# Performance work log

Measured on AMD Instinct MI355X. Metric: run time of the kernel, lower is better.

The kernel has to match this reference:

```python
import jax, jax.numpy as jnp
import numpy as np

DISCRETIZATION = "IM"  # matches init_kwargs


def setup_inputs() -> dict:
    key = jax.random.key(0)
    ks = jax.random.split(key, 6)
    Bt, L, H, P = 16, 4096, 128, 256
    std = 1.0 / np.sqrt(H)
    return {
        "inputs": jax.random.normal(ks[0], (Bt, L, H), jnp.float32),
        "A_diag": jax.random.uniform(ks[1], (P,), jnp.float32, 0.0, 1.0),
        "B": jax.random.uniform(ks[2], (P, H, 2), jnp.float32, -std, std),
        "C": jax.random.uniform(ks[3], (H, P, 2), jnp.float32, -std, std),
        "D": jax.random.normal(ks[4], (H,), jnp.float32),
        "steps": jax.random.uniform(ks[5], (P,), jnp.float32, 0.0, 1.0),
    }


def _combine(l, r):
    # 2x2 block composition: new_A = r.A @ l.A ; new_b = r.A @ l.b + r.b
    la11, la12, la21, la22, lb1, lb2 = l
    ra11, ra12, ra21, ra22, rb1, rb2 = r
    c11 = ra11 * la11 + ra12 * la21
    c12 = ra11 * la12 + ra12 * la22
    c21 = ra21 * la11 + ra22 * la21
    c22 = ra21 * la12 + ra22 * la22
    nb1 = ra11 * lb1 + ra12 * lb2 + rb1
    nb2 = ra21 * lb1 + ra22 * lb2 + rb2
    return (c11, c12, c21, c22, nb1, nb2)


def reference(inputs, A_diag, B, C, D, steps):
    Bt, L, H = inputs.shape
    P = A_diag.shape[0]
    a = jax.nn.relu(A_diag)                 # (P,)
    step = jax.nn.sigmoid(steps)            # (P,)
    Bc = jax.lax.complex(B[..., 0], B[..., 1])   # (P, H) complex64
    Cc = jax.lax.complex(C[..., 0], C[..., 1])   # (H, P) complex64

    # bu = inputs @ B^T  -> (Bt, L, P), complex
    bu = jnp.einsum("blh,ph->blp", inputs.astype(jnp.complex64), Bc)

    if DISCRETIZATION == "IM":
        s2a = step * step * a
        schur = 1.0 / (1.0 + s2a)
        m11 = 1.0 - s2a * schur
        m12 = -step * a * schur
        m21 = step * schur
        m22 = schur
        f1 = (m11 * step) * bu
        f2 = (m21 * step) * bu
    else:  # IMEX
        m11 = jnp.ones_like(a)
        m12 = -step * a
        m21 = step
        m22 = 1.0 - step * step * a
        f1 = bu * step
        f2 = bu * (step * step)

    # sequence axis leading for the scan: (L, Bt, P)
    f1 = jnp.moveaxis(f1, 1, 0)
    f2 = jnp.moveaxis(f2, 1, 0)
    # time-invariant 2x2 per-channel blocks, broadcast to (L, 1, P) complex
    a_elems = tuple(
        jnp.broadcast_to(m.astype(jnp.complex64)[None, None, :], (L, 1, P))
        for m in (m11, m12, m21, m22)
    )
    _, _, _, _, _x1, x2 = jax.lax.associative_scan(
        _combine, (*a_elems, f1, f2), axis=0
    )
    states = x2  # (L, Bt, P): position component (index 1 of 2x2 state)

    projected = jnp.einsum("lbp,hp->blh", states, Cc).real  # (Bt, L, H)
    return projected + inputs * D
```

## Files before the change

kernel.cpp:

```cpp
#include <hip/hip_runtime.h>
#include <math.h>


constexpr int BTc = 16;
constexpr int Lc  = 4096;
constexpr int Hc  = 128;
constexpr int Pc  = 256;
constexpr int CL  = 64;
constexpr int NC  = Lc / CL;
constexpr int LOG2CL = 6;

typedef __attribute__((ext_vector_type(8))) short short8;
typedef __attribute__((ext_vector_type(4))) float f32x4;

constexpr size_t CF_OFF  = 0;
constexpr size_t BF_OFF  = 16384;
constexpr size_t CFR_OFF = BF_OFF + 131072;
constexpr size_t LOC_OFF = CFR_OFF + 131072;
constexpr size_t INI_OFF = LOC_OFF + 4194304;

constexpr int LDS_U   = 0;
constexpr int LDS_BUX = 16384;
constexpr int LDS_BYTES = 81920;

__device__ __forceinline__ unsigned short f2bf(float x) {
    unsigned u = __float_as_uint(x);
    u += 0x7fffu + ((u >> 16) & 1u);
    return (unsigned short)(u >> 16);
}
__device__ __forceinline__ float bf2f(unsigned short h) {
    return __uint_as_float(((unsigned)h) << 16);
}
__device__ __forceinline__ f32x4 mfma16(short8 a, short8 b, f32x4 c) {
    return __builtin_amdgcn_mfma_f32_16x16x32_bf16(a, b, c, 0, 0, 0);
}
__device__ __forceinline__ int swz(int l) { return (l ^ (l >> 3)) & 7; }

__global__ __launch_bounds__(256) void k_prep(const float* __restrict__ A_diag,
                                              const float* __restrict__ steps,
                                              const float* __restrict__ Bw,
                                              const float* __restrict__ Cw,
                                              float* __restrict__ cf,
                                              unsigned short* __restrict__ BF,
                                              unsigned short* __restrict__ CFr) {
    int idx = blockIdx.x * 256 + threadIdx.x;
    {
        int j = idx & 7, lane = (idx >> 3) & 63, nfg = (idx >> 9) & 31, kt = idx >> 14;
        int k = kt * 32 + (lane >> 4) * 8 + j;
        int n = nfg * 16 + (lane & 15);
        int p = n >> 1, part = n & 1;
        BF[idx] = f2bf(Bw[(p * Hc + k) * 2 + part]);
    }
    {
        int j = idx & 7, lane = (idx >> 3) & 63, nfg = (idx >> 9) & 7, ktG = idx >> 12;
        int k = ktG * 32 + (lane >> 4) * 8 + j;
        int h = nfg * 16 + (lane & 15);
        int p = k >> 1, part = k & 1;
        float v = Cw[(h * Pc + p) * 2 + part];
        CFr[idx] = f2bf(part ? -v : v);
    }
    if (blockIdx.x == 0) {
        int p = threadIdx.x;
        float a  = fmaxf(A_diag[p], 0.0f);
        float st = 1.0f / (1.0f + expf(-steps[p]));
        float s2a   = st * st * a;
        float schur = 1.0f / (1.0f + s2a);
        float m11 = 1.0f - s2a * schur;
        float m12 = -st * a * schur;
        float m21 = st * schur;
        float m22 = schur;
        cf[0*Pc+p] = m11;  cf[1*Pc+p] = m12;
        cf[2*Pc+p] = m21;  cf[3*Pc+p] = m22;
        cf[4*Pc+p] = m11 * st;
        cf[5*Pc+p] = m21 * st;
        float a11=m11, a12=m12, a21=m21, a22=m22;
        #pragma unroll
        for (int i = 0; i < LOG2CL; i++) {
            float b11 = a11*a11 + a12*a21;
            float b12 = a11*a12 + a12*a22;
            float b21 = a21*a11 + a22*a21;
            float b22 = a21*a12 + a22*a22;
            a11=b11; a12=b12; a21=b21; a22=b22;
        }
        cf[6*Pc+p]=a11; cf[7*Pc+p]=a12; cf[8*Pc+p]=a21; cf[9*Pc+p]=a22;
    }
}

__global__ __launch_bounds__(512) void k_scanB(const float* __restrict__ cf,
                                               const float2* __restrict__ loc,
                                               float2* __restrict__ ini) {
    int b = blockIdx.x, n = threadIdx.x;
    int p = n >> 1;
    float A11=cf[6*Pc+p], A12=cf[7*Pc+p], A21=cf[8*Pc+p], A22=cf[9*Pc+p];
    float x1 = 0.f, x2 = 0.f;
    for (int g = 0; g < 8; g++) {
        float2 lv[8];
        #pragma unroll
        for (int j = 0; j < 8; j++)
            lv[j] = loc[((size_t)(b * NC + g * 8 + j)) * 512 + n];
        #pragma unroll
        for (int j = 0; j < 8; j++) {
            size_t idx = ((size_t)(b * NC + g * 8 + j)) * 512 + n;
            ini[idx] = make_float2(x1, x2);
            float n1 = fmaf(A11, x1, fmaf(A12, x2, lv[j].x));
            float n2 = fmaf(A21, x1, fmaf(A22, x2, lv[j].y));
            x1 = n1; x2 = n2;
        }
    }
}

template<int PASS>
__global__ __launch_bounds__(512, 4) void k_pass(const float* __restrict__ in,
                                                 const float* __restrict__ cf,
                                                 const unsigned short* __restrict__ BF,
                                                 const unsigned short* __restrict__ CFr,
                                                 const float* __restrict__ Dw,
                                                 float2* __restrict__ loc,
                                                 const float2* __restrict__ ini,
                                                 float* __restrict__ out) {
    __shared__ float4 smem4[LDS_BYTES / 16];
    char* sm = (char*)smem4;

    int tid  = threadIdx.x;
    int lane = tid & 63;
    int w    = tid >> 6;
    int wm   = w >> 2, wn = w & 3;
    int bc   = blockIdx.x;
    size_t mbase = (size_t)bc * CL;
    int r = lane & 15, q = lane >> 4;

    {
        int l   = tid >> 3;
        int kc0 = (tid & 7) * 2;
        const float* g = in + (mbase + l) * Hc + (tid & 7) * 16;
        float4 f0 = *(const float4*)(g);
        float4 f1 = *(const float4*)(g + 4);
        float4 f2 = *(const float4*)(g + 8);
        float4 f3 = *(const float4*)(g + 12);
        short8 c0, c1;
        c0[0]=(short)f2bf(f0.x); c0[1]=(short)f2bf(f0.y); c0[2]=(short)f2bf(f0.z); c0[3]=(short)f2bf(f0.w);
        c0[4]=(short)f2bf(f1.x); c0[5]=(short)f2bf(f1.y); c0[6]=(short)f2bf(f1.z); c0[7]=(short)f2bf(f1.w);
        c1[0]=(short)f2bf(f2.x); c1[1]=(short)f2bf(f2.y); c1[2]=(short)f2bf(f2.z); c1[3]=(short)f2bf(f2.w);
        c1[4]=(short)f2bf(f3.x); c1[5]=(short)f2bf(f3.y); c1[6]=(short)f2bf(f3.z); c1[7]=(short)f2bf(f3.w);
        int sw = l & 7;
        *(short8*)(sm + LDS_U + l * 256 + (((kc0    ) ^ sw) << 4)) = c0;
        *(short8*)(sm + LDS_U + l * 256 + (((kc0 + 1) ^ sw) << 4)) = c1;
    }
    __syncthreads();

    #pragma unroll
    for (int half = 0; half < 2; ++half) {
        f32x4 acc[2][4];
        #pragma unroll
        for (int i = 0; i < 2; i++)
            #pragma unroll
            for (int j = 0; j < 4; j++) acc[i][j] = (f32x4)(0.0f);

        #pragma unroll
        for (int kt = 0; kt < 4; ++kt) {
            short8 a[2];
            #pragma unroll
            for (int mf = 0; mf < 2; ++mf) {
                int la = wm * 32 + mf * 16 + r;
                int kc = kt * 4 + q;
                a[mf] = *(const short8*)(sm + LDS_U + la * 256 + ((kc ^ (la & 7)) << 4));
            }
            #pragma unroll
            for (int nfi = 0; nfi < 4; ++nfi) {
                int nfg = half * 16 + wn * 4 + nfi;
                short8 bb = *(const short8*)(BF + (size_t)((kt * 32 + nfg) * 64 + lane) * 8);
                acc[0][nfi] = mfma16(a[0], bb, acc[0][nfi]);
                acc[1][nfi] = mfma16(a[1], bb, acc[1][nfi]);
            }
        }
        char* bux = sm + LDS_BUX + half * 32768;
        #pragma unroll
        for (int mf = 0; mf < 2; ++mf)
            #pragma unroll
            for (int nfi = 0; nfi < 4; ++nfi) {
                int nn = wn * 64 + nfi * 16 + r;
                int kc = nn >> 3, e = nn & 7;
                #pragma unroll
                for (int j = 0; j < 4; ++j) {
                    int l = wm * 32 + mf * 16 + q * 4 + j;
                    *(unsigned short*)(bux + l * 512 + ((kc ^ swz(l)) << 4) + e * 2)
                        = f2bf(acc[mf][nfi][j]);
                }
            }
    }
    __syncthreads();

    {
        int ng = tid, h = ng >> 8, n = ng & 255, p = ng >> 1;
        float m11 = cf[p],        m12 = cf[256 + p];
        float m21 = cf[512 + p],  m22 = cf[768 + p];
        float s1  = cf[1024 + p], s2  = cf[1280 + p];
        float x1, x2;
        if constexpr (PASS == 1) { x1 = 0.f; x2 = 0.f; }
        else { float2 iv = ini[(size_t)bc * 512 + ng]; x1 = iv.x; x2 = iv.y; }
        char* bux = sm + LDS_BUX + h * 32768 + (n & 7) * 2;
        int kc = n >> 3;
        #pragma unroll 4
        for (int l = 0; l < CL; ++l) {
            char* addr = bux + l * 512 + ((kc ^ swz(l)) << 4);
            float f  = bf2f(*(unsigned short*)addr);
            float n1 = fmaf(m11, x1, fmaf(m12, x2, s1 * f));
            float n2 = fmaf(m21, x1, fmaf(m22, x2, s2 * f));
            x1 = n1; x2 = n2;
            if constexpr (PASS == 2) *(unsigned short*)addr = f2bf(x2);
        }
        if constexpr (PASS == 1) loc[(size_t)bc * 512 + ng] = make_float2(x1, x2);
    }

    if constexpr (PASS == 2) {
        __syncthreads();
        f32x4 acc2[2][2];
        #pragma unroll
        for (int i = 0; i < 2; i++)
            #pragma unroll
            for (int j = 0; j < 2; j++) acc2[i][j] = (f32x4)(0.0f);

        #pragma unroll
        for (int half = 0; half < 2; ++half) {
            char* bux = sm + LDS_BUX + half * 32768;
            #pragma unroll
            for (int kt = 0; kt < 8; ++kt) {
                short8 a2[2];
                #pragma unroll
                for (int mf = 0; mf < 2; ++mf) {
                    int la  = wm * 32 + mf * 16 + r;
                    int kc2 = kt * 4 + q;
                    a2[mf] = *(const short8*)(bux + la * 512 + ((kc2 ^ swz(la)) << 4));
                }
                #pragma unroll
                for (int nfi = 0; nfi < 2; ++nfi) {
                    int ktG = half * 8 + kt;
                    int nfg = wn * 2 + nfi;
                    short8 bb = *(const short8*)(CFr + (size_t)((ktG * 8 + nfg) * 64 + lane) * 8);
                    acc2[0][nfi] = mfma16(a2[0], bb, acc2[0][nfi]);
                    acc2[1][nfi] = mfma16(a2[1], bb, acc2[1][nfi]);
                }
            }
        }
        #pragma unroll
        for (int nfi = 0; nfi < 2; ++nfi) {
            int h = wn * 32 + nfi * 16 + r;
            float d = Dw[h];
            #pragma unroll
            for (int mf = 0; mf < 2; ++mf)
                #pragma unroll
                for (int j = 0; j < 4; ++j) {
                    int l = wm * 32 + mf * 16 + q * 4 + j;
                    size_t gm = mbase + l;
                    out[gm * Hc + h] = fmaf(in[gm * Hc + h], d, acc2[mf][nfi][j]);
                }
        }
    }
}

extern "C" void kernel_launch(void* const* d_in, const int* in_sizes, int n_in,
                              void* d_out, int out_size, void* d_ws, size_t ws_size,
                              hipStream_t stream) {
    const float* in  = (const float*)d_in[0];
    const float* Ad  = (const float*)d_in[1];
    const float* Bw  = (const float*)d_in[2];
    const float* Cw  = (const float*)d_in[3];
    const float* Dw  = (const float*)d_in[4];
    const float* stp = (const float*)d_in[5];
    char* ws = (char*)d_ws;
    float*          cf  = (float*)(ws + CF_OFF);
    unsigned short* BF  = (unsigned short*)(ws + BF_OFF);
    unsigned short* CFr = (unsigned short*)(ws + CFR_OFF);
    float2*         loc = (float2*)(ws + LOC_OFF);
    float2*         ini = (float2*)(ws + INI_OFF);
    float* out = (float*)d_out;

    k_prep<<<256, 256, 0, stream>>>(Ad, stp, Bw, Cw, cf, BF, CFr);
    k_pass<1><<<BTc * NC, 512, 0, stream>>>(in, cf, BF, CFr, Dw, loc, ini, out);
    k_scanB<<<BTc, 512, 0, stream>>>(cf, loc, ini);
    k_pass<2><<<BTc * NC, 512, 0, stream>>>(in, cf, BF, CFr, Dw, loc, ini, out);
}
```

Measured before the change: 150.9 us.

## Replace first-pass sequential chunk scan with weighted-sum reduction and halve pass-two LDS

```diff
diff --git a/kernel.cpp b/kernel.cpp
--- a/kernel.cpp
+++ b/kernel.cpp
@@ -15,13 +15,16 @@
 
 constexpr size_t CF_OFF  = 0;
 constexpr size_t BF_OFF  = 16384;
-constexpr size_t CFR_OFF = BF_OFF + 131072;
-constexpr size_t LOC_OFF = CFR_OFF + 131072;
+constexpr size_t CFR_OFF = BF_OFF  + 131072;
+constexpr size_t W_OFF   = CFR_OFF + 131072;
+constexpr size_t LOC_OFF = W_OFF   + 131072;
 constexpr size_t INI_OFF = LOC_OFF + 4194304;
 
 constexpr int LDS_U   = 0;
 constexpr int LDS_BUX = 16384;
-constexpr int LDS_BYTES = 81920;
+constexpr int LDS2_BYTES = 49152;
+constexpr int LDS_PART = 16384;
+constexpr int LDSS_BYTES = 20480;
 
 __device__ __forceinline__ unsigned short f2bf(float x) {
     unsigned u = __float_as_uint(x);
@@ -42,7 +45,8 @@
                                               const float* __restrict__ Cw,
                                               float* __restrict__ cf,
                                               unsigned short* __restrict__ BF,
-                                              unsigned short* __restrict__ CFr) {
+                                              unsigned short* __restrict__ CFr,
+                                              float2* __restrict__ W) {
     int idx = blockIdx.x * 256 + threadIdx.x;
     {
         int j = idx & 7, lane = (idx >> 3) & 63, nfg = (idx >> 9) & 31, kt = idx >> 14;
@@ -71,8 +75,16 @@
         float m22 = schur;
         cf[0*Pc+p] = m11;  cf[1*Pc+p] = m12;
         cf[2*Pc+p] = m21;  cf[3*Pc+p] = m22;
-        cf[4*Pc+p] = m11 * st;
-        cf[5*Pc+p] = m21 * st;
+        float s1 = m11 * st, s2 = m21 * st;
+        cf[4*Pc+p] = s1;
+        cf[5*Pc+p] = s2;
+        float w1 = s1, w2 = s2;
+        for (int k = 0; k < CL; k++) {
+            W[p * CL + k] = make_float2(w1, w2);
+            float t1 = fmaf(m11, w1, m12 * w2);
+            float t2 = fmaf(m21, w1, m22 * w2);
+            w1 = t1; w2 = t2;
+        }
         float a11=m11, a12=m12, a21=m21, a22=m22;
         #pragma unroll
         for (int i = 0; i < LOG2CL; i++) {
@@ -109,17 +121,59 @@
     }
 }
 
-template<int PASS>
-__global__ __launch_bounds__(512, 4) void k_pass(const float* __restrict__ in,
-                                                 const float* __restrict__ cf,
-                                                 const unsigned short* __restrict__ BF,
-                                                 const unsigned short* __restrict__ CFr,
-                                                 const float* __restrict__ Dw,
-                                                 float2* __restrict__ loc,
-                                                 const float2* __restrict__ ini,
-                                                 float* __restrict__ out) {
-    __shared__ float4 smem4[LDS_BYTES / 16];
+__device__ __forceinline__ void stage_U(char* sm, const float* __restrict__ in,
+                                        size_t mbase, int tid) {
+    int l   = tid >> 3;
+    int kc0 = (tid & 7) * 2;
+    const float* g = in + (mbase + l) * Hc + (tid & 7) * 16;
+    float4 f0 = *(const float4*)(g);
+    float4 f1 = *(const float4*)(g + 4);
+    float4 f2 = *(const float4*)(g + 8);
+    float4 f3 = *(const float4*)(g + 12);
+    short8 c0, c1;
+    c0[0]=(short)f2bf(f0.x); c0[1]=(short)f2bf(f0.y); c0[2]=(short)f2bf(f0.z); c0[3]=(short)f2bf(f0.w);
+    c0[4]=(short)f2bf(f1.x); c0[5]=(short)f2bf(f1.y); c0[6]=(short)f2bf(f1.z); c0[7]=(short)f2bf(f1.w);
+    c1[0]=(short)f2bf(f2.x); c1[1]=(short)f2bf(f2.y); c1[2]=(short)f2bf(f2.z); c1[3]=(short)f2bf(f2.w);
+    c1[4]=(short)f2bf(f3.x); c1[5]=(short)f2bf(f3.y); c1[6]=(short)f2bf(f3.z); c1[7]=(short)f2bf(f3.w);
+    int sw = l & 7;
+    *(short8*)(sm + LDS_U + l * 256 + (((kc0    ) ^ sw) << 4)) = c0;
+    *(short8*)(sm + LDS_U + l * 256 + (((kc0 + 1) ^ sw) << 4)) = c1;
+}
+
+__device__ __forceinline__ void gemm1_half(char* sm, const unsigned short* __restrict__ BF,
+                                           int half, int wm, int wn, int lane,
+                                           f32x4 (&acc)[2][4]) {
+    int r = lane & 15, q = lane >> 4;
+    #pragma unroll
+    for (int i = 0; i < 2; i++)
+        #pragma unroll
+        for (int j = 0; j < 4; j++) acc[i][j] = (f32x4)(0.0f);
+    #pragma unroll
+    for (int kt = 0; kt < 4; ++kt) {
+        short8 a[2];
+        #pragma unroll
+        for (int mf = 0; mf < 2; ++mf) {
+            int la = wm * 32 + mf * 16 + r;
+            int kc = kt * 4 + q;
+            a[mf] = *(const short8*)(sm + LDS_U + la * 256 + ((kc ^ (la & 7)) << 4));
+        }
+        #pragma unroll
+        for (int nfi = 0; nfi < 4; ++nfi) {
+            int nfg = half * 16 + wn * 4 + nfi;
+            short8 bb = *(const short8*)(BF + (size_t)((kt * 32 + nfg) * 64 + lane) * 8);
+            acc[0][nfi] = mfma16(a[0], bb, acc[0][nfi]);
+            acc[1][nfi] = mfma16(a[1], bb, acc[1][nfi]);
+        }
+    }
+}
+
+__global__ __launch_bounds__(512, 6) void k_sum(const float* __restrict__ in,
+                                                const unsigned short* __restrict__ BF,
+                                                const float2* __restrict__ W,
+                                                float2* __restrict__ loc) {
+    __shared__ float4 smem4[LDSS_BYTES / 16];
     char* sm = (char*)smem4;
+    float2* part = (float2*)(sm + LDS_PART);
 
     int tid  = threadIdx.x;
     int lane = tid & 63;
@@ -129,51 +183,85 @@
     size_t mbase = (size_t)bc * CL;
     int r = lane & 15, q = lane >> 4;
 
-    {
-        int l   = tid >> 3;
-        int kc0 = (tid & 7) * 2;
-        const float* g = in + (mbase + l) * Hc + (tid & 7) * 16;
-        float4 f0 = *(const float4*)(g);
-        float4 f1 = *(const float4*)(g + 4);
-        float4 f2 = *(const float4*)(g + 8);
-        float4 f3 = *(const float4*)(g + 12);
-        short8 c0, c1;
-        c0[0]=(short)f2bf(f0.x); c0[1]=(short)f2bf(f0.y); c0[2]=(short)f2bf(f0.z); c0[3]=(short)f2bf(f0.w);
-        c0[4]=(short)f2bf(f1.x); c0[5]=(short)f2bf(f1.y); c0[6]=(short)f2bf(f1.z); c0[7]=(short)f2bf(f1.w);
-        c1[0]=(short)f2bf(f2.x); c1[1]=(short)f2bf(f2.y); c1[2]=(short)f2bf(f2.z); c1[3]=(short)f2bf(f2.w);
-        c1[4]=(short)f2bf(f3.x); c1[5]=(short)f2bf(f3.y); c1[6]=(short)f2bf(f3.z); c1[7]=(short)f2bf(f3.w);
-        int sw = l & 7;
-        *(short8*)(sm + LDS_U + l * 256 + (((kc0    ) ^ sw) << 4)) = c0;
-        *(short8*)(sm + LDS_U + l * 256 + (((kc0 + 1) ^ sw) << 4)) = c1;
-    }
+    stage_U(sm, in, mbase, tid);
     __syncthreads();
 
     #pragma unroll
     for (int half = 0; half < 2; ++half) {
         f32x4 acc[2][4];
-        #pragma unroll
-        for (int i = 0; i < 2; i++)
-            #pragma unroll
-            for (int j = 0; j < 4; j++) acc[i][j] = (f32x4)(0.0f);
-
-        #pragma unroll
-        for (int kt = 0; kt < 4; ++kt) {
-            short8 a[2];
-            #pragma unroll
-            for (int mf = 0; mf < 2; ++mf) {
-                int la = wm * 32 + mf * 16 + r;
-                int kc = kt * 4 + q;
-                a[mf] = *(const short8*)(sm + LDS_U + la * 256 + ((kc ^ (la & 7)) << 4));
-            }
-            #pragma unroll
-            for (int nfi = 0; nfi < 4; ++nfi) {
-                int nfg = half * 16 + wn * 4 + nfi;
-                short8 bb = *(const short8*)(BF + (size_t)((kt * 32 + nfg) * 64 + lane) * 8);
-                acc[0][nfi] = mfma16(a[0], bb, acc[0][nfi]);
-                acc[1][nfi] = mfma16(a[1], bb, acc[1][nfi]);
-            }
-        }
-        char* bux = sm + LDS_BUX + half * 32768;
+        gemm1_half(sm, BF, half, wm, wn, lane, acc);
+
+        float P1[4], P2[4];
+        #pragma unroll
+        for (int nfi = 0; nfi < 4; ++nfi) { P1[nfi] = 0.f; P2[nfi] = 0.f; }
+        #pragma unroll
+        for (int mf = 0; mf < 2; ++mf)
+            #pragma unroll
+            for (int j = 0; j < 4; ++j) {
+                int l = wm * 32 + mf * 16 + q * 4 + j;
+                #pragma unroll
+                for (int nfi = 0; nfi < 4; ++nfi) {
+                    int p = half * 128 + wn * 32 + nfi * 8 + (r >> 1);
+                    float2 wv = W[p * CL + (CL - 1 - l)];
+                    P1[nfi] = fmaf(wv.x, acc[mf][nfi][j], P1[nfi]);
+                    P2[nfi] = fmaf(wv.y, acc[mf][nfi][j], P2[nfi]);
+                }
+            }
+        #pragma unroll
+        for (int nfi = 0; nfi < 4; ++nfi) {
+            P1[nfi] += __shfl_xor(P1[nfi], 16);
+            P1[nfi] += __shfl_xor(P1[nfi], 32);
+            P2[nfi] += __shfl_xor(P2[nfi], 16);
+            P2[nfi] += __shfl_xor(P2[nfi], 32);
+        }
+        if (lane < 16) {
+            #pragma unroll
+            for (int nfi = 0; nfi < 4; ++nfi)
+                part[wm * 256 + wn * 64 + nfi * 16 + r] = make_float2(P1[nfi], P2[nfi]);
+        }
+        __syncthreads();
+        if (tid < 256) {
+            float2 a = part[tid], b = part[256 + tid];
+            loc[(size_t)bc * 512 + half * 256 + tid] = make_float2(a.x + b.x, a.y + b.y);
+        }
+        __syncthreads();
+    }
+}
+
+__global__ __launch_bounds__(512, 6) void k_pass2(const float* __restrict__ in,
+                                                  const float* __restrict__ cf,
+                                                  const unsigned short* __restrict__ BF,
+                                                  const unsigned short* __restrict__ CFr,
+                                                  const float* __restrict__ Dw,
+                                                  const float2* __restrict__ ini,
+                                                  float* __restrict__ out) {
+    __shared__ float4 smem4[LDS2_BYTES / 16];
+    char* sm = (char*)smem4;
+    char* bux = sm + LDS_BUX;
+
+    int tid  = threadIdx.x;
+    int lane = tid & 63;
+    int w    = tid >> 6;
+    int wm   = w >> 2, wn = w & 3;
+    int bc   = blockIdx.x;
+    size_t mbase = (size_t)bc * CL;
+    int r = lane & 15, q = lane >> 4;
+
+    stage_U(sm, in, mbase, tid);
+    __syncthreads();
+
+    f32x4 acc2[2][2];
+    #pragma unroll
+    for (int i = 0; i < 2; i++)
+        #pragma unroll
+        for (int j = 0; j < 2; j++) acc2[i][j] = (f32x4)(0.0f);
+
+    #pragma unroll
+    for (int half = 0; half < 2; ++half) {
+        f32x4 acc[2][4];
+        gemm1_half(sm, BF, half, wm, wn, lane, acc);
+
+        __syncthreads();
         #pragma unroll
         for (int mf = 0; mf < 2; ++mf)
             #pragma unroll
@@ -187,74 +275,61 @@
                         = f2bf(acc[mf][nfi][j]);
                 }
             }
-    }
-    __syncthreads();
-
-    {
-        int ng = tid, h = ng >> 8, n = ng & 255, p = ng >> 1;
-        float m11 = cf[p],        m12 = cf[256 + p];
-        float m21 = cf[512 + p],  m22 = cf[768 + p];
-        float s1  = cf[1024 + p], s2  = cf[1280 + p];
-        float x1, x2;
-        if constexpr (PASS == 1) { x1 = 0.f; x2 = 0.f; }
-        else { float2 iv = ini[(size_t)bc * 512 + ng]; x1 = iv.x; x2 = iv.y; }
-        char* bux = sm + LDS_BUX + h * 32768 + (n & 7) * 2;
-        int kc = n >> 3;
-        #pragma unroll 4
-        for (int l = 0; l < CL; ++l) {
-            char* addr = bux + l * 512 + ((kc ^ swz(l)) << 4);
-            float f  = bf2f(*(unsigned short*)addr);
-            float n1 = fmaf(m11, x1, fmaf(m12, x2, s1 * f));
-            float n2 = fmaf(m21, x1, fmaf(m22, x2, s2 * f));
-            x1 = n1; x2 = n2;
-            if constexpr (PASS == 2) *(unsigned short*)addr = f2bf(x2);
-        }
-        if constexpr (PASS == 1) loc[(size_t)bc * 512 + ng] = make_float2(x1, x2);
-    }
-
-    if constexpr (PASS == 2) {
-        __syncthreads();
-        f32x4 acc2[2][2];
-        #pragma unroll
-        for (int i = 0; i < 2; i++)
-            #pragma unroll
-            for (int j = 0; j < 2; j++) acc2[i][j] = (f32x4)(0.0f);
-
-        #pragma unroll
-        for (int half = 0; half < 2; ++half) {
-            char* bux = sm + LDS_BUX + half * 32768;
-            #pragma unroll
-            for (int kt = 0; kt < 8; ++kt) {
-                short8 a2[2];
-                #pragma unroll
-                for (int mf = 0; mf < 2; ++mf) {
-                    int la  = wm * 32 + mf * 16 + r;
-                    int kc2 = kt * 4 + q;
-                    a2[mf] = *(const short8*)(bux + la * 512 + ((kc2 ^ swz(la)) << 4));
-                }
-                #pragma unroll
-                for (int nfi = 0; nfi < 2; ++nfi) {
-                    int ktG = half * 8 + kt;
-                    int nfg = wn * 2 + nfi;
-                    short8 bb = *(const short8*)(CFr + (size_t)((ktG * 8 + nfg) * 64 + lane) * 8);
-                    acc2[0][nfi] = mfma16(a2[0], bb, acc2[0][nfi]);
-                    acc2[1][nfi] = mfma16(a2[1], bb, acc2[1][nfi]);
-                }
-            }
-        }
-        #pragma unroll
-        for (int nfi = 0; nfi < 2; ++nfi) {
-            int h = wn * 32 + nfi * 16 + r;
-            float d = Dw[h];
-            #pragma unroll
-            for (int mf = 0; mf < 2; ++mf)
-                #pragma unroll
-                for (int j = 0; j < 4; ++j) {
-                    int l = wm * 32 + mf * 16 + q * 4 + j;
-                    size_t gm = mbase + l;
-                    out[gm * Hc + h] = fmaf(in[gm * Hc + h], d, acc2[mf][nfi][j]);
-                }
-        }
+        __syncthreads();
+
+        if (tid < 256) {
+            int n = tid, ng = half * 256 + n, p = ng >> 1;
+            float m11 = cf[p],        m12 = cf[256 + p];
+            float m21 = cf[512 + p],  m22 = cf[768 + p];
+            float s1  = cf[1024 + p], s2  = cf[1280 + p];
+            float2 iv = ini[(size_t)bc * 512 + ng];
+            float x1 = iv.x, x2 = iv.y;
+            char* bp = bux + (n & 7) * 2;
+            int kc = n >> 3;
+            #pragma unroll 4
+            for (int l = 0; l < CL; ++l) {
+                char* addr = bp + l * 512 + ((kc ^ swz(l)) << 4);
+                float f  = bf2f(*(unsigned short*)addr);
+                float n1 = fmaf(m11, x1, fmaf(m12, x2, s1 * f));
+                float n2 = fmaf(m21, x1, fmaf(m22, x2, s2 * f));
+                x1 = n1; x2 = n2;
+                *(unsigned short*)addr = f2bf(x2);
+            }
+        }
+        __syncthreads();
+
+        #pragma unroll
+        for (int kt = 0; kt < 8; ++kt) {
+            short8 a2[2];
+            #pragma unroll
+            for (int mf = 0; mf < 2; ++mf) {
+                int la  = wm * 32 + mf * 16 + r;
+                int kc2 = kt * 4 + q;
+                a2[mf] = *(const short8*)(bux + la * 512 + ((kc2 ^ swz(la)) << 4));
+            }
+            #pragma unroll
+            for (int nfi = 0; nfi < 2; ++nfi) {
+                int ktG = half * 8 + kt;
+                int nfg = wn * 2 + nfi;
+                short8 bb = *(const short8*)(CFr + (size_t)((ktG * 8 + nfg) * 64 + lane) * 8);
+                acc2[0][nfi] = mfma16(a2[0], bb, acc2[0][nfi]);
+                acc2[1][nfi] = mfma16(a2[1], bb, acc2[1][nfi]);
+            }
+        }
+    }
+
+    #pragma unroll
+    for (int nfi = 0; nfi < 2; ++nfi) {
+        int h = wn * 32 + nfi * 16 + r;
+        float d = Dw[h];
+        #pragma unroll
+        for (int mf = 0; mf < 2; ++mf)
+            #pragma unroll
+            for (int j = 0; j < 4; ++j) {
+                int l = wm * 32 + mf * 16 + q * 4 + j;
+                size_t gm = mbase + l;
+                out[gm * Hc + h] = fmaf(in[gm * Hc + h], d, acc2[mf][nfi][j]);
+            }
     }
 }
 
@@ -271,12 +346,13 @@
     float*          cf  = (float*)(ws + CF_OFF);
     unsigned short* BF  = (unsigned short*)(ws + BF_OFF);
     unsigned short* CFr = (unsigned short*)(ws + CFR_OFF);
+    float2*         W   = (float2*)(ws + W_OFF);
     float2*         loc = (float2*)(ws + LOC_OFF);
     float2*         ini = (float2*)(ws + INI_OFF);
     float* out = (float*)d_out;
 
-    k_prep<<<256, 256, 0, stream>>>(Ad, stp, Bw, Cw, cf, BF, CFr);
-    k_pass<1><<<BTc * NC, 512, 0, stream>>>(in, cf, BF, CFr, Dw, loc, ini, out);
+    k_prep<<<256, 256, 0, stream>>>(Ad, stp, Bw, Cw, cf, BF, CFr, W);
+    k_sum<<<BTc * NC, 512, 0, stream>>>(in, BF, W, loc);
     k_scanB<<<BTc, 512, 0, stream>>>(cf, loc, ini);
-    k_pass<2><<<BTc * NC, 512, 0, stream>>>(in, cf, BF, CFr, Dw, loc, ini, out);
-}
+    k_pass2<<<BTc * NC, 512, 0, stream>>>(in, cf, BF, CFr, Dw, ini, out);
+}
```

Measured after the change: 210.8 us. +39.7%, slower.
